# Optimization experiments

Measured on AMD Instinct MI355X. Metric: run time of the kernel, lower is better.

The kernel has to match this reference:

```python
import jax, jax.numpy as jnp
import numpy as np

KY, KX = 3, 3  # kernel_size from init_kwargs


def setup_inputs() -> dict:
    key = jax.random.key(0)
    x = jax.random.normal(key, (8, 32, 512, 512), dtype=jnp.float32)
    return {"x": x}


def reference(x):
    # Replicate-pad H by (KY-1)//2, W by (KX-1)//2 (matches F.pad mode='replicate').
    py, px = (KY - 1) // 2, (KX - 1) // 2
    B, C, H, W = x.shape
    padded = jnp.pad(x, ((0, 0), (0, 0), (py, py), (px, px)), mode='edge')
    center = (KY * KX) // 2
    # The torch module builds an identity neigh2channel kernel with the center
    # tap zeroed, then maxes over the KY*KX channels. The zeroed center channel
    # contributes a constant 0 to that max, so we initialize the running max at 0
    # and fold in every non-center neighbor via shifted slices (no blown-up
    # [B,C,KY*KX,H,W] tensor is materialized).
    m = jnp.zeros_like(x)
    for idx in range(KY * KX):
        if idx == center:
            continue
        i, j = divmod(idx, KX)
        m = jnp.maximum(m, padded[:, :, i:i + H, j:j + W])
    mask = (x > m).astype(x.dtype)
    return x * mask
```

## Files before the change

kernel.cpp:

```cpp
#include <hip/hip_runtime.h>


#define IMG_W 512
#define IMG_H 512
#define NPLANES 256
#define CHUNK 64
#define THREADS 256
#define WAVES_PER_BLOCK (THREADS / 64)
#define CHUNKS_PER_PLANE (IMG_H / CHUNK)

typedef float v4f __attribute__((ext_vector_type(4)));

static_assert(IMG_W == 64 * 8, "one wave covers a full row at 8 floats/lane");
static_assert(IMG_H % CHUNK == 0, "chunks divide evenly");

__device__ __forceinline__ void load_row(const float* __restrict__ base, int r,
                                         float d[8]) {
    const v4f a = *(const v4f*)(base + (size_t)r * IMG_W);
    const v4f b = *(const v4f*)(base + (size_t)r * IMG_W + 4);
    d[0] = a.x; d[1] = a.y; d[2] = a.z; d[3] = a.w;
    d[4] = b.x; d[5] = b.y; d[6] = b.z; d[7] = b.w;
}

__device__ __forceinline__ void row_stats(const float d[8], int lane,
                                          float lr[8], float hm[8]) {
    float lnb = __shfl_up(d[7], 1);
    lnb = (lane == 0) ? d[0] : lnb;
    float rnb = __shfl_down(d[0], 1);
    rnb = (lane == 63) ? d[7] : rnb;

    lr[0] = fmaxf(lnb,  d[1]);
    lr[1] = fmaxf(d[0], d[2]);
    lr[2] = fmaxf(d[1], d[3]);
    lr[3] = fmaxf(d[2], d[4]);
    lr[4] = fmaxf(d[3], d[5]);
    lr[5] = fmaxf(d[4], d[6]);
    lr[6] = fmaxf(d[5], d[7]);
    lr[7] = fmaxf(d[6], rnb);
#pragma unroll
    for (int i = 0; i < 8; ++i) hm[i] = fmaxf(lr[i], d[i]);
}

__global__ __launch_bounds__(THREADS)
void nms3x3_kernel(const float* __restrict__ x, float* __restrict__ out) {
    const int wid   = blockIdx.x * WAVES_PER_BLOCK + (threadIdx.x >> 6);
    const int lane  = threadIdx.x & 63;
    const int plane = wid / CHUNKS_PER_PLANE;
    const int chunk = wid % CHUNKS_PER_PLANE;
    const int r0    = chunk * CHUNK;

    const float* img  = x   + (size_t)plane * IMG_H * IMG_W + lane * 8;
    float*       oimg = out + (size_t)plane * IMG_H * IMG_W + lane * 8;

    float pd[8], cd[8], nd[8];
    float pHm[8], cLr[8], cHm[8], nLr[8], nHm[8];
    float junk[8];

    load_row(img, (r0 > 0) ? r0 - 1 : 0, pd);
    row_stats(pd, lane, junk, pHm);
    load_row(img, r0, cd);
    row_stats(cd, lane, cLr, cHm);

    for (int k = 0; k < CHUNK; ++k) {
        const int r  = r0 + k;
        const int rn = (r + 1 < IMG_H) ? r + 1 : IMG_H - 1;
        load_row(img, rn, nd);
        row_stats(nd, lane, nLr, nHm);

        float o[8];
#pragma unroll
        for (int i = 0; i < 8; ++i) {
            float m = fmaxf(fmaxf(pHm[i], nHm[i]), cLr[i]);
            m = fmaxf(m, 0.0f);
            o[i] = (cd[i] > m) ? cd[i] : 0.0f;
        }

        v4f oa = { o[0], o[1], o[2], o[3] };
        v4f ob = { o[4], o[5], o[6], o[7] };
        __builtin_nontemporal_store(oa, (v4f*)(oimg + (size_t)r * IMG_W));
        __builtin_nontemporal_store(ob, (v4f*)(oimg + (size_t)r * IMG_W + 4));

#pragma unroll
        for (int i = 0; i < 8; ++i) {
            pHm[i] = cHm[i];
            cd[i]  = nd[i];
            cLr[i] = nLr[i];
            cHm[i] = nHm[i];
        }
    }
}

extern "C" void kernel_launch(void* const* d_in, const int* in_sizes, int n_in,
                              void* d_out, int out_size, void* d_ws, size_t ws_size,
                              hipStream_t stream) {
    const float* x = (const float*)d_in[0];
    float* out     = (float*)d_out;
    const int total_waves = NPLANES * CHUNKS_PER_PLANE;
    dim3 grid(total_waves / WAVES_PER_BLOCK);
    nms3x3_kernel<<<grid, dim3(THREADS), 0, stream>>>(x, out);
}
```

Before: 466.6 us.

## Prefetch rows through a 4-deep register ring with full unroll and smaller chunks

```diff
diff --git a/kernel.cpp b/kernel.cpp
--- a/kernel.cpp
+++ b/kernel.cpp
@@ -4,7 +4,7 @@
 #define IMG_W 512
 #define IMG_H 512
 #define NPLANES 256
-#define CHUNK 64
+#define CHUNK 32
 #define THREADS 256
 #define WAVES_PER_BLOCK (THREADS / 64)
 #define CHUNKS_PER_PLANE (IMG_H / CHUNK)
@@ -13,17 +13,18 @@
 
 static_assert(IMG_W == 64 * 8, "one wave covers a full row at 8 floats/lane");
 static_assert(IMG_H % CHUNK == 0, "chunks divide evenly");
+static_assert(CHUNK % 4 == 0, "ring phase aligned across chunks");
 
 __device__ __forceinline__ void load_row(const float* __restrict__ base, int r,
-                                         float d[8]) {
+                                         float (&d)[8]) {
     const v4f a = *(const v4f*)(base + (size_t)r * IMG_W);
     const v4f b = *(const v4f*)(base + (size_t)r * IMG_W + 4);
     d[0] = a.x; d[1] = a.y; d[2] = a.z; d[3] = a.w;
     d[4] = b.x; d[5] = b.y; d[6] = b.z; d[7] = b.w;
 }
 
-__device__ __forceinline__ void row_stats(const float d[8], int lane,
-                                          float lr[8], float hm[8]) {
+__device__ __forceinline__ void row_stats(const float (&d)[8], int lane,
+                                          float (&lr)[8], float (&hm)[8]) {
     float lnb = __shfl_up(d[7], 1);
     lnb = (lane == 0) ? d[0] : lnb;
     float rnb = __shfl_down(d[0], 1);
@@ -41,7 +42,7 @@
     for (int i = 0; i < 8; ++i) hm[i] = fmaxf(lr[i], d[i]);
 }
 
-__global__ __launch_bounds__(THREADS)
+__global__ __launch_bounds__(THREADS, 4)
 void nms3x3_kernel(const float* __restrict__ x, float* __restrict__ out) {
     const int wid   = blockIdx.x * WAVES_PER_BLOCK + (threadIdx.x >> 6);
     const int lane  = threadIdx.x & 63;
@@ -52,41 +53,46 @@
     const float* img  = x   + (size_t)plane * IMG_H * IMG_W + lane * 8;
     float*       oimg = out + (size_t)plane * IMG_H * IMG_W + lane * 8;
 
-    float pd[8], cd[8], nd[8];
-    float pHm[8], cLr[8], cHm[8], nLr[8], nHm[8];
-    float junk[8];
+    float rowd[4][8];
+    float hmR[4][8];
+    float lrR[2][8];
 
-    load_row(img, (r0 > 0) ? r0 - 1 : 0, pd);
-    row_stats(pd, lane, junk, pHm);
-    load_row(img, r0, cd);
-    row_stats(cd, lane, cLr, cHm);
+    load_row(img, (r0 > 0) ? r0 - 1 : 0, rowd[3]);
+    load_row(img, r0,     rowd[0]);
+    load_row(img, r0 + 1, rowd[1]);
+    load_row(img, r0 + 2, rowd[2]);
+    {
+        float junk[8];
+        row_stats(rowd[3], lane, junk, hmR[3]);
+    }
+    row_stats(rowd[0], lane, lrR[0], hmR[0]);
 
+#pragma unroll
     for (int k = 0; k < CHUNK; ++k) {
-        const int r  = r0 + k;
-        const int rn = (r + 1 < IMG_H) ? r + 1 : IMG_H - 1;
-        load_row(img, rn, nd);
-        row_stats(nd, lane, nLr, nHm);
+        const int r = r0 + k;
+
+        if (k < CHUNK - 2) {
+            int rf = r + 3;
+            rf = (rf < IMG_H) ? rf : IMG_H - 1;
+            load_row(img, rf, rowd[(k + 3) & 3]);
+        }
+
+        row_stats(rowd[(k + 1) & 3], lane, lrR[(k + 1) & 1], hmR[(k + 1) & 3]);
 
         float o[8];
 #pragma unroll
         for (int i = 0; i < 8; ++i) {
-            float m = fmaxf(fmaxf(pHm[i], nHm[i]), cLr[i]);
+            float m = fmaxf(fmaxf(hmR[(k + 3) & 3][i], hmR[(k + 1) & 3][i]),
+                            lrR[k & 1][i]);
             m = fmaxf(m, 0.0f);
-            o[i] = (cd[i] > m) ? cd[i] : 0.0f;
+            const float c = rowd[k & 3][i];
+            o[i] = (c > m) ? c : 0.0f;
         }
 
-        v4f oa = { o[0], o[1], o[2], o[3] };
-        v4f ob = { o[4], o[5], o[6], o[7] };
+        const v4f oa = { o[0], o[1], o[2], o[3] };
+        const v4f ob = { o[4], o[5], o[6], o[7] };
         __builtin_nontemporal_store(oa, (v4f*)(oimg + (size_t)r * IMG_W));
         __builtin_nontemporal_store(ob, (v4f*)(oimg + (size_t)r * IMG_W + 4));
-
-#pragma unroll
-        for (int i = 0; i < 8; ++i) {
-            pHm[i] = cHm[i];
-            cd[i]  = nd[i];
-            cLr[i] = nLr[i];
-            cHm[i] = nHm[i];
-        }
     }
 }
 
```

After: 483.3 us. 3.6% more time.
